# Kernel optimization log

Hardware: AMD Instinct MI355X
Metric: run time of the kernel (lower is better)

Reference implementation:

```python
import jax, jax.numpy as jnp
import numpy as np

MG = (5, 5)          # mesh_grid_size
UP = (17, 17)        # upsample_size
IMG = (512.0, 512.0) # image_size
B = 8192
FC_OUT = MG[0] * MG[1] * 2  # 50
KH = (UP[0] - 1) // (MG[0] - 1) + 1  # 5
KW = (UP[1] - 1) // (MG[1] - 1) + 1  # 5
SH = (UP[0] - 1) // (MG[0] - 1)      # 4
SW = (UP[1] - 1) // (MG[1] - 1)      # 4
L0 = MG[0] - 1
L1 = MG[1] - 1


def _grid(h, w):
    # channel 0: x coords vary along rows (image_size[0]); channel 1: y along cols
    x_t = jnp.broadcast_to(jnp.linspace(0.0, IMG[0], h)[:, None], (h, w))
    y_t = jnp.broadcast_to(jnp.linspace(0.0, IMG[1], w)[None, :], (h, w))
    return jnp.stack([x_t, y_t], 0)  # [2, h, w]


def _unfold22(a):
    # a: [B, 2, H, W] -> [B, (H-1)*(W-1), 4, 2]; 4 = kernel positions row-major, 2 = channel
    p = jnp.stack([a[:, :, :-1, :-1], a[:, :, :-1, 1:],
                   a[:, :, 1:, :-1], a[:, :, 1:, 1:]], axis=2)  # [B,2,4,H-1,W-1]
    return p.reshape(a.shape[0], 2, 4, -1).transpose(0, 3, 2, 1)


def _persp(src, dst):
    # exact 4-point homography solve (torchgeometry.get_perspective_transform)
    x0, y0 = src[..., 0], src[..., 1]
    u, v = dst[..., 0], dst[..., 1]
    z = jnp.zeros_like(x0)
    o = jnp.ones_like(x0)
    ax = jnp.stack([x0, y0, o, z, z, z, -u * x0, -u * y0], -1)  # [N,4,8]
    ay = jnp.stack([z, z, z, x0, y0, o, -v * x0, -v * y0], -1)
    A = jnp.concatenate([ax, ay], 1)                 # [N,8,8]
    bb = jnp.concatenate([u, v], 1)[..., None]       # [N,8,1]
    h = jnp.linalg.solve(A, bb)[..., 0]              # [N,8]
    return jnp.concatenate([h, o[:, :1]], 1).reshape(-1, 3, 3)


def setup_inputs() -> dict:
    key = jax.random.key(0)
    ks = jax.random.split(key, 4)
    def lin(k, i, o):
        return jax.random.normal(k, (i, o), jnp.float32) / jnp.sqrt(i)
    return {
        "x": jax.random.normal(ks[0], (B, 1024), jnp.float32),
        "W1": lin(ks[1], 1024, 1024), "b1": jnp.zeros((1024,), jnp.float32),
        "W2": lin(ks[2], 1024, 2048), "b2": jnp.zeros((2048,), jnp.float32),
        "W3": lin(ks[3], 2048, FC_OUT), "b3": jnp.zeros((FC_OUT,), jnp.float32),
    }


def reference(x, W1, b1, W2, b2, W3, b3):
    Bn = x.shape[0]
    h = jax.nn.relu(x @ W1 + b1)
    h = jax.nn.relu(h @ W2 + b2)
    out = (h @ W3 + b3).reshape(Bn, 2, MG[0], MG[1])  # [B,2,5,5] mesh flow

    # sparse control grid and 2x2 patch corner points
    gs = _grid(MG[0], MG[1])
    src = _unfold22(jnp.broadcast_to(gs[None], (Bn, 2, MG[0], MG[1]))).reshape(-1, 4, 2)
    flow = _unfold22(out).reshape(-1, 4, 2)
    M = _persp(src, src + flow)  # [B*16, 3, 3]

    # dense grid and its unfold2 (kernel KHxKW, stride SHxSW) patch points
    gd = _grid(UP[0], UP[1])  # [2, 17, 17]
    gi = (np.arange(L0) * SH)[:, None, None, None] + np.arange(KH)[None, None, :, None]
    gj = (np.arange(L1) * SW)[None, :, None, None] + np.arange(KW)[None, None, None, :]
    I, J = np.broadcast_arrays(gi, gj)  # [L0,L1,KH,KW]
    pts = gd[:, I, J].transpose(1, 2, 3, 4, 0).reshape(1, L0 * L1, KH * KW, 2)
    pts = jnp.broadcast_to(pts, (Bn, L0 * L1, KH * KW, 2)).reshape(Bn * L0 * L1, KH * KW, 2)

    # transform_points: homogeneous warp + perspective divide
    ph = jnp.concatenate([pts, jnp.ones(pts.shape[:-1] + (1,), pts.dtype)], -1)
    oh = jnp.einsum('nij,npj->npi', M, ph)
    warped = oh[..., :2] / oh[..., 2:3]
    warped = warped.reshape(Bn, L0, L1, KH, KW, 2)

    # Fold: scatter-accumulate overlapping patches
    fold = jnp.zeros((Bn, 2, UP[0], UP[1]), x.dtype)
    for i in range(L0):
        for j in range(L1):
            blk = warped[:, i, j].transpose(0, 3, 1, 2)  # [B,2,KH,KW]
            fold = fold.at[:, :, i * SH:i * SH + KH, j * SW:j * SW + KW].add(blk)

    # boundary rescaling exactly as the torch code: only the 5x5 crossing points
    idx = np.arange(0, UP[0], MG[0] - 1)
    X, Y = np.meshgrid(idx, idx, indexing='xy')
    fold = fold.at[:, :, X, Y].multiply(0.5)
    for (a, b) in ((0, 0), (0, UP[1] - 1), (UP[0] - 1, UP[1] - 1), (UP[0] - 1, 0)):
        fold = fold.at[:, :, a, b].multiply(2.0)

    return fold - gd[None]  # upsampled mesh flow [B,2,17,17]
```

## Files before the change

### kernel.cpp

```cpp
#include <hip/hip_runtime.h>

typedef __bf16 bf16x8 __attribute__((ext_vector_type(8)));
typedef float f32x4 __attribute__((ext_vector_type(4)));

__device__ __forceinline__ unsigned short f2bf(float f) {
  unsigned int u = __builtin_bit_cast(unsigned int, f);
  unsigned int r = (u + 0x7fffu + ((u >> 16) & 1u)) >> 16;
  return (unsigned short)r;
}

__device__ __forceinline__ float bf2f(unsigned short u) {
  unsigned int v = ((unsigned int)u) << 16;
  return __builtin_bit_cast(float, v);
}

__device__ __forceinline__ void load16_lds(const unsigned short* g, unsigned short* l) {
  __builtin_amdgcn_global_load_lds(
      (const __attribute__((address_space(1))) void*)g,
      (__attribute__((address_space(3))) void*)l, 16, 0, 0);
}

__device__ __forceinline__ void wait_vm0() {
  asm volatile("s_waitcnt vmcnt(0)" ::: "memory");
  __builtin_amdgcn_sched_barrier(0);
}
__device__ __forceinline__ void barrier_raw() {
  __builtin_amdgcn_sched_barrier(0);
  __builtin_amdgcn_s_barrier();
  __builtin_amdgcn_sched_barrier(0);
}


__global__ __launch_bounds__(256) void prepass(
    const float* __restrict__ x, const float* __restrict__ W1,
    const float* __restrict__ W2, const float* __restrict__ W3,
    unsigned short* __restrict__ xbf, unsigned short* __restrict__ w1t,
    unsigned short* __restrict__ w2t, unsigned short* __restrict__ w3t) {
  __shared__ float tile[32][33];
  const int bid = blockIdx.x;
  const int t = threadIdx.x;
  if (bid < 2048) {
    for (int i = bid * 256 + t; i < 2097152; i += 2048 * 256) {
      float4 f = ((const float4*)x)[i];
      uint2 o;
      o.x = (unsigned)f2bf(f.x) | ((unsigned)f2bf(f.y) << 16);
      o.y = (unsigned)f2bf(f.z) | ((unsigned)f2bf(f.w) << 16);
      ((uint2*)xbf)[i] = o;
    }
  } else if (bid < 3072) {
    int ti = bid - 2048;
    int n0 = (ti & 31) * 32, k0 = (ti >> 5) * 32;
    int tx = t & 31, ty = t >> 5;
    #pragma unroll
    for (int r = 0; r < 32; r += 8)
      tile[ty + r][tx] = W1[(size_t)(k0 + ty + r) * 1024 + n0 + tx];
    __syncthreads();
    #pragma unroll
    for (int r = 0; r < 32; r += 8)
      w1t[(size_t)(n0 + ty + r) * 1024 + k0 + tx] = f2bf(tile[tx][ty + r]);
  } else if (bid < 5120) {
    int ti = bid - 3072;
    int n0 = (ti & 63) * 32, k0 = (ti >> 6) * 32;
    int tx = t & 31, ty = t >> 5;
    #pragma unroll
    for (int r = 0; r < 32; r += 8)
      tile[ty + r][tx] = W2[(size_t)(k0 + ty + r) * 2048 + n0 + tx];
    __syncthreads();
    #pragma unroll
    for (int r = 0; r < 32; r += 8)
      w2t[(size_t)(n0 + ty + r) * 1024 + k0 + tx] = f2bf(tile[tx][ty + r]);
  } else {
    int idx = (bid - 5120) * 256 + t;
    int n = idx >> 11, k = idx & 2047;
    w3t[idx] = f2bf((n < 50) ? W3[(size_t)k * 50 + n] : 0.f);
  }
}


__global__ __launch_bounds__(256, 2) void gemm1_v8(
    const unsigned short* __restrict__ A,
    const unsigned short* __restrict__ Bt,
    const float* __restrict__ bias,
    unsigned short* __restrict__ C) {
  constexpr int K = 1024, N = 1024, NT = 16;
  constexpr int AEL = 128 * 64;
  constexpr int BUF = 2 * AEL;
  __shared__ __align__(16) unsigned short smem[2 * BUF];
  const int t = threadIdx.x;
  const int m0 = blockIdx.x * 128;
  const int n0 = blockIdx.y * 128;
  const int lane = t & 63, wv = t >> 6;
  const int l16 = lane & 15, quad = lane >> 4;
  const int rb = (wv >> 1) * 64, cb = (wv & 1) * 64;

  const int srow = t >> 3;
  const int sg = ((t & 7) ^ (srow & 7)) * 8;
  const unsigned short* Ag0 = A + (size_t)(m0 + srow) * K + sg;
  const unsigned short* Bg0 = Bt + (size_t)(n0 + srow) * K + sg;
  const int ldsO = wv * 8 * 64;

  f32x4 acc[4][4] = {};

  #pragma unroll
  for (int r = 0; r < 4; ++r) {
    load16_lds(Ag0 + (size_t)(r * 32) * K, &smem[r * 2048 + ldsO]);
    load16_lds(Bg0 + (size_t)(r * 32) * K, &smem[AEL + r * 2048 + ldsO]);
  }

  for (int kt = 0; kt < NT; ++kt) {
    unsigned short* Ls = &smem[(kt & 1) * BUF];

    wait_vm0();
    barrier_raw();

    if (kt + 1 < NT) {
      unsigned short* Ln = &smem[((kt + 1) & 1) * BUF];
      const unsigned short* An = Ag0 + (size_t)(kt + 1) * 64;
      const unsigned short* Bn = Bg0 + (size_t)(kt + 1) * 64;
      #pragma unroll
      for (int r = 0; r < 4; ++r) {
        load16_lds(An + (size_t)(r * 32) * K, &Ln[r * 2048 + ldsO]);
        load16_lds(Bn + (size_t)(r * 32) * K, &Ln[AEL + r * 2048 + ldsO]);
      }
    }

    #pragma unroll
    for (int half = 0; half < 2; ++half) {
      bf16x8 af[4], bfr[4];
      #pragma unroll
      for (int ni = 0; ni < 4; ++ni) {
        int row = cb + ni * 16 + l16;
        bfr[ni] = *(const bf16x8*)&Ls[AEL + row * 64 + ((half * 4 + quad) ^ (row & 7)) * 8];
      }
      #pragma unroll
      for (int mi = 0; mi < 4; ++mi) {
        int row = rb + mi * 16 + l16;
        af[mi] = *(const bf16x8*)&Ls[row * 64 + ((half * 4 + quad) ^ (row & 7)) * 8];
      }
      #pragma unroll
      for (int mi = 0; mi < 4; ++mi)
        #pragma unroll
        for (int ni = 0; ni < 4; ++ni)
          acc[mi][ni] = __builtin_amdgcn_mfma_f32_16x16x32_bf16(
              af[mi], bfr[ni], acc[mi][ni], 0, 0, 0);
    }
  }
  barrier_raw();

  unsigned short* Cs = smem;
  float bv[4];
  #pragma unroll
  for (int ni = 0; ni < 4; ++ni) bv[ni] = bias[n0 + cb + ni * 16 + l16];
  #pragma unroll
  for (int mi = 0; mi < 4; ++mi)
    #pragma unroll
    for (int ni = 0; ni < 4; ++ni)
      #pragma unroll
      for (int r = 0; r < 4; ++r) {
        int row = rb + mi * 16 + quad * 4 + r;
        int col = cb + ni * 16 + l16;
        int pb = (col >> 3) ^ (row & 15);
        Cs[row * 128 + pb * 8 + (col & 7)] = f2bf(fmaxf(acc[mi][ni][r] + bv[ni], 0.f));
      }
  __syncthreads();
  #pragma unroll
  for (int j = 0; j < 8; ++j) {
    int idx = j * 256 + t;
    int row = idx >> 4, cg = idx & 15;
    int pb = cg ^ (row & 15);
    *(uint4*)&C[(size_t)(m0 + row) * N + n0 + cg * 8] =
        *(const uint4*)&Cs[row * 128 + pb * 8];
  }
}


__global__ __launch_bounds__(512, 4) void gemm2_v8(
    const unsigned short* __restrict__ A,
    const unsigned short* __restrict__ Bt,
    const float* __restrict__ bias,
    const unsigned short* __restrict__ W3t,
    unsigned short* __restrict__ part) {
  constexpr int K = 1024, NT = 32;
  constexpr int AEL = 256 * 32;
  constexpr int BEL = 128 * 32;
  constexpr int BUF = AEL + BEL;
  __shared__ __align__(16) unsigned short smem[32768];
  const int t = threadIdx.x;
  const int m0 = blockIdx.x * 256;
  const int n0 = blockIdx.y * 128;
  const int lane = t & 63, wv = t >> 6;
  const int l16 = lane & 15, quad = lane >> 4;
  const int rb = (wv >> 1) * 64, cb = (wv & 1) * 64;

  const int tr = t >> 2;
  const int cg = ((t & 3) - (tr >> 1)) & 3;
  const unsigned short* Ag0 = A + (size_t)(m0 + tr) * K + cg * 8;
  const unsigned short* Bg0 = Bt + (size_t)(n0 + tr) * K + cg * 8;
  const int ldsO = wv * 512;

  f32x4 acc[4][4] = {};

  load16_lds(Ag0, &smem[ldsO]);
  load16_lds(Ag0 + (size_t)128 * K, &smem[4096 + ldsO]);
  load16_lds(Bg0, &smem[AEL + ldsO]);

  for (int kt = 0; kt < NT; ++kt) {
    unsigned short* Ls = &smem[(kt & 1) * BUF];

    wait_vm0();
    barrier_raw();

    if (kt + 1 < NT) {
      unsigned short* Ln = &smem[((kt + 1) & 1) * BUF];
      const unsigned short* An = Ag0 + (size_t)(kt + 1) * 32;
      const unsigned short* Bn = Bg0 + (size_t)(kt + 1) * 32;
      load16_lds(An, &Ln[ldsO]);
      load16_lds(An + (size_t)128 * K, &Ln[4096 + ldsO]);
      load16_lds(Bn, &Ln[AEL + ldsO]);
    }

    bf16x8 af[4], bfr[4];
    #pragma unroll
    for (int ni = 0; ni < 4; ++ni) {
      int row = cb + ni * 16 + l16;
      bfr[ni] = *(const bf16x8*)&Ls[AEL + row * 32 + ((quad + (row >> 1)) & 3) * 8];
    }
    #pragma unroll
    for (int mi = 0; mi < 4; ++mi) {
      int row = rb + mi * 16 + l16;
      af[mi] = *(const bf16x8*)&Ls[row * 32 + ((quad + (row >> 1)) & 3) * 8];
    }
    #pragma unroll
    for (int mi = 0; mi < 4; ++mi)
      #pragma unroll
      for (int ni = 0; ni < 4; ++ni)
        acc[mi][ni] = __builtin_amdgcn_mfma_f32_16x16x32_bf16(
            af[mi], bfr[ni], acc[mi][ni], 0, 0, 0);
  }
  barrier_raw();

  unsigned short* Cs = smem;
  float bv[4];
  #pragma unroll
  for (int ni = 0; ni < 4; ++ni) bv[ni] = bias[n0 + cb + ni * 16 + l16];
  #pragma unroll
  for (int mi = 0; mi < 4; ++mi)
    #pragma unroll
    for (int ni = 0; ni < 4; ++ni)
      #pragma unroll
      for (int r = 0; r < 4; ++r) {
        int row = rb + mi * 16 + quad * 4 + r;
        int col = cb + ni * 16 + l16;
        int pb = (col >> 3) ^ (row & 15);
        Cs[row * 128 + pb * 8 + (col & 7)] = f2bf(fmaxf(acc[mi][ni][r] + bv[ni], 0.f));
      }
  __syncthreads();

  bf16x8 bq[4][4];
  #pragma unroll
  for (int ks = 0; ks < 4; ++ks)
    #pragma unroll
    for (int nt = 0; nt < 4; ++nt)
      bq[ks][nt] = *(const bf16x8*)&W3t[(size_t)(nt * 16 + l16) * 2048 +
                                        n0 + ks * 32 + quad * 8];
  f32x4 acc2[2][4] = {};
  #pragma unroll
  for (int ks = 0; ks < 4; ++ks) {
    bf16x8 af2[2];
    #pragma unroll
    for (int mt = 0; mt < 2; ++mt) {
      int row = wv * 32 + mt * 16 + l16;
      int pb = (ks * 4 + quad) ^ (row & 15);
      af2[mt] = *(const bf16x8*)&Cs[row * 128 + pb * 8];
    }
    #pragma unroll
    for (int mt = 0; mt < 2; ++mt)
      #pragma unroll
      for (int nt = 0; nt < 4; ++nt)
        acc2[mt][nt] = __builtin_amdgcn_mfma_f32_16x16x32_bf16(
            af2[mt], bq[ks][nt], acc2[mt][nt], 0, 0, 0);
  }

  const int zi = blockIdx.y;
  #pragma unroll
  for (int mt = 0; mt < 2; ++mt)
    #pragma unroll
    for (int nt = 0; nt < 4; ++nt) {
      int col = nt * 16 + l16;
      #pragma unroll
      for (int r = 0; r < 4; ++r) {
        int row = m0 + wv * 32 + mt * 16 + quad * 4 + r;
        part[((size_t)row * 16 + zi) * 64 + col] = f2bf(acc2[mt][nt][r]);
      }
    }
}


__global__ __launch_bounds__(256) void geom_reduce(
    const unsigned short* __restrict__ part,
    const float* __restrict__ b3,
    float* __restrict__ outp) {
  __shared__ float s_out3[16 * 64];
  __shared__ float unfold[16][16][50];
  const int t = threadIdx.x;
  const int bbase = blockIdx.x * 16;

  for (int i = t; i < 1024; i += 256) {
    int m = i >> 6, n = i & 63;
    const unsigned short* p = part + ((size_t)(bbase + m) * 16) * 64 + n;
    float v = 0.f;
    #pragma unroll
    for (int z = 0; z < 16; ++z) v += bf2f(p[z * 64]);
    s_out3[i] = v + ((n < 50) ? b3[n] : 0.f);
  }
  __syncthreads();

  {
    const int bl = t >> 4;
    const int p = t & 15;
    const int pi = p >> 2, pj = p & 3;
    const float* o = &s_out3[bl * 64];

    float u00 = 128.f * pi       + o[pi * 5 + pj];
    float v00 = 128.f * pj       + o[25 + pi * 5 + pj];
    float u01 = 128.f * pi       + o[pi * 5 + pj + 1];
    float v01 = 128.f * (pj + 1) + o[25 + pi * 5 + pj + 1];
    float u10 = 128.f * (pi + 1) + o[(pi + 1) * 5 + pj];
    float v10 = 128.f * pj       + o[25 + (pi + 1) * 5 + pj];
    float u11 = 128.f * (pi + 1) + o[(pi + 1) * 5 + pj + 1];
    float v11 = 128.f * (pj + 1) + o[25 + (pi + 1) * 5 + pj + 1];

    float sx = u00 - u10 + u11 - u01;
    float sy = v00 - v10 + v11 - v01;
    float dx1 = u10 - u11, dx2 = u01 - u11;
    float dy1 = v10 - v11, dy2 = v01 - v11;
    float rden = 1.f / (dx1 * dy2 - dx2 * dy1);
    float g = (sx * dy2 - dx2 * sy) * rden;
    float h = (dx1 * sy - sx * dy1) * rden;
    float a = u10 - u00 + g * u10;
    float b = u01 - u00 + h * u01;
    float c = u00;
    float d = v10 - v00 + g * v10;
    float e = v01 - v00 + h * v01;
    float f = v00;

    #pragma unroll
    for (int ai = 0; ai < 5; ++ai) {
      #pragma unroll
      for (int bi = 0; bi < 5; ++bi) {
        float s = 0.25f * ai, tt = 0.25f * bi;
        float rw = 1.f / (g * s + h * tt + 1.f);
        unfold[bl][p][ai * 5 + bi]      = (a * s + b * tt + c) * rw;
        unfold[bl][p][25 + ai * 5 + bi] = (d * s + e * tt + f) * rw;
      }
    }
  }
  __syncthreads();

  for (int i = t; i < 16 * 578; i += 256) {
    int blb = i / 578;
    int rem = i - blb * 578;
    int ch = rem / 289;
    int ij = rem - ch * 289;
    int gi = ij / 17, gj = ij - gi * 17;

    int pi0 = (gi == 16) ? 3 : (gi >> 2);
    int ai0 = gi - 4 * pi0;
    int ci = (((gi & 3) == 0) && gi != 0 && gi != 16) ? 2 : 1;
    int pj0 = (gj == 16) ? 3 : (gj >> 2);
    int bj0 = gj - 4 * pj0;
    int cj = (((gj & 3) == 0) && gj != 0 && gj != 16) ? 2 : 1;

    float val = 0.f;
    #pragma unroll
    for (int ii = 0; ii < 2; ++ii) {
      if (ii < ci) {
        int pi = pi0 - ii, ai = ii ? 4 : ai0;
        #pragma unroll
        for (int jj = 0; jj < 2; ++jj) {
          if (jj < cj) {
            int pj = pj0 - jj, bi = jj ? 4 : bj0;
            val += unfold[blb][pi * 4 + pj][ch * 25 + ai * 5 + bi];
          }
        }
      }
    }

    if (((gi & 3) == 0) && ((gj & 3) == 0)) val *= 0.5f;
    if ((gi == 0 || gi == 16) && (gj == 0 || gj == 16)) val *= 2.f;
    val -= (ch == 0) ? 32.f * gi : 32.f * gj;
    outp[(size_t)(bbase + blb) * 578 + rem] = val;
  }
}


extern "C" void kernel_launch(void* const* d_in, const int* in_sizes, int n_in,
                              void* d_out, int out_size, void* d_ws, size_t ws_size,
                              hipStream_t stream) {
  const float* x  = (const float*)d_in[0];
  const float* W1 = (const float*)d_in[1];
  const float* b1 = (const float*)d_in[2];
  const float* W2 = (const float*)d_in[3];
  const float* b2 = (const float*)d_in[4];
  const float* W3 = (const float*)d_in[5];
  const float* b3 = (const float*)d_in[6];
  float* outp = (float*)d_out;

  char* ws = (char*)d_ws;
  unsigned short* xbf = (unsigned short*)ws;
  unsigned short* w1t = (unsigned short*)(ws + (size_t)16 * 1024 * 1024);
  unsigned short* part = (unsigned short*)ws;
  unsigned short* w2t = (unsigned short*)(ws + (size_t)34 * 1024 * 1024);
  unsigned short* w3t = (unsigned short*)(ws + (size_t)38 * 1024 * 1024);
  unsigned short* h1  = (unsigned short*)(ws + (size_t)38 * 1024 * 1024 + 512 * 1024);

  prepass<<<5632, 256, 0, stream>>>(x, W1, W2, W3, xbf, w1t, w2t, w3t);

  gemm1_v8<<<dim3(64, 8), 256, 0, stream>>>(xbf, w1t, b1, h1);
  gemm2_v8<<<dim3(32, 16), 512, 0, stream>>>(h1, w2t, b2, w3t, part);
  geom_reduce<<<512, 256, 0, stream>>>(part, b3, outp);
}
```

Before: 184.1 us.

## Restructure gemm1 to 512 threads with K-tile 32 and new LDS swizzle

Rewrites the first GEMM kernel to use 512 threads per block (8 waves, each computing 32x64) instead of 256 threads (4 waves, 64x64). The K tile drops from 64 to 32, so LDS per block halves and the kernel runs twice as many K iterations, with a new rotation-based LDS swizzle. The intent is more waves in flight and higher occupancy to hide memory latency. In exchange each wave reuses fewer A fragments per B load, and there are twice as many barriers per block.

Result: no change. 181.5 us (-1.4%).

```diff
diff --git a/kernel.cpp b/kernel.cpp
--- a/kernel.cpp
+++ b/kernel.cpp
@@ -77,13 +77,13 @@
 }
 
 
-__global__ __launch_bounds__(256, 2) void gemm1_v8(
+__global__ __launch_bounds__(512, 4) void gemm1_v9(
     const unsigned short* __restrict__ A,
     const unsigned short* __restrict__ Bt,
     const float* __restrict__ bias,
     unsigned short* __restrict__ C) {
-  constexpr int K = 1024, N = 1024, NT = 16;
-  constexpr int AEL = 128 * 64;
+  constexpr int K = 1024, N = 1024, NT = 32;
+  constexpr int AEL = 128 * 32;
   constexpr int BUF = 2 * AEL;
   __shared__ __align__(16) unsigned short smem[2 * BUF];
   const int t = threadIdx.x;
@@ -91,21 +91,18 @@
   const int n0 = blockIdx.y * 128;
   const int lane = t & 63, wv = t >> 6;
   const int l16 = lane & 15, quad = lane >> 4;
-  const int rb = (wv >> 1) * 64, cb = (wv & 1) * 64;
-
-  const int srow = t >> 3;
-  const int sg = ((t & 7) ^ (srow & 7)) * 8;
-  const unsigned short* Ag0 = A + (size_t)(m0 + srow) * K + sg;
-  const unsigned short* Bg0 = Bt + (size_t)(n0 + srow) * K + sg;
-  const int ldsO = wv * 8 * 64;
-
-  f32x4 acc[4][4] = {};
-
-  #pragma unroll
-  for (int r = 0; r < 4; ++r) {
-    load16_lds(Ag0 + (size_t)(r * 32) * K, &smem[r * 2048 + ldsO]);
-    load16_lds(Bg0 + (size_t)(r * 32) * K, &smem[AEL + r * 2048 + ldsO]);
-  }
+  const int rb = (wv >> 1) * 32, cb = (wv & 1) * 64;
+
+  const int tr = t >> 2;
+  const int cg = ((t & 3) - (tr >> 1)) & 3;
+  const unsigned short* Ag0 = A + (size_t)(m0 + tr) * K + cg * 8;
+  const unsigned short* Bg0 = Bt + (size_t)(n0 + tr) * K + cg * 8;
+  const int ldsO = wv * 512;
+
+  f32x4 acc[2][4] = {};
+
+  load16_lds(Ag0, &smem[ldsO]);
+  load16_lds(Bg0, &smem[AEL + ldsO]);
 
   for (int kt = 0; kt < NT; ++kt) {
     unsigned short* Ls = &smem[(kt & 1) * BUF];
@@ -115,35 +112,27 @@
 
     if (kt + 1 < NT) {
       unsigned short* Ln = &smem[((kt + 1) & 1) * BUF];
-      const unsigned short* An = Ag0 + (size_t)(kt + 1) * 64;
-      const unsigned short* Bn = Bg0 + (size_t)(kt + 1) * 64;
-      #pragma unroll
-      for (int r = 0; r < 4; ++r) {
-        load16_lds(An + (size_t)(r * 32) * K, &Ln[r * 2048 + ldsO]);
-        load16_lds(Bn + (size_t)(r * 32) * K, &Ln[AEL + r * 2048 + ldsO]);
-      }
-    }
-
-    #pragma unroll
-    for (int half = 0; half < 2; ++half) {
-      bf16x8 af[4], bfr[4];
-      #pragma unroll
-      for (int ni = 0; ni < 4; ++ni) {
-        int row = cb + ni * 16 + l16;
-        bfr[ni] = *(const bf16x8*)&Ls[AEL + row * 64 + ((half * 4 + quad) ^ (row & 7)) * 8];
-      }
-      #pragma unroll
-      for (int mi = 0; mi < 4; ++mi) {
-        int row = rb + mi * 16 + l16;
-        af[mi] = *(const bf16x8*)&Ls[row * 64 + ((half * 4 + quad) ^ (row & 7)) * 8];
-      }
-      #pragma unroll
-      for (int mi = 0; mi < 4; ++mi)
-        #pragma unroll
-        for (int ni = 0; ni < 4; ++ni)
-          acc[mi][ni] = __builtin_amdgcn_mfma_f32_16x16x32_bf16(
-              af[mi], bfr[ni], acc[mi][ni], 0, 0, 0);
-    }
+      load16_lds(Ag0 + (size_t)(kt + 1) * 32, &Ln[ldsO]);
+      load16_lds(Bg0 + (size_t)(kt + 1) * 32, &Ln[AEL + ldsO]);
+    }
+
+    bf16x8 af[2], bfr[4];
+    #pragma unroll
+    for (int ni = 0; ni < 4; ++ni) {
+      int row = cb + ni * 16 + l16;
+      bfr[ni] = *(const bf16x8*)&Ls[AEL + row * 32 + ((quad + (row >> 1)) & 3) * 8];
+    }
+    #pragma unroll
+    for (int mi = 0; mi < 2; ++mi) {
+      int row = rb + mi * 16 + l16;
+      af[mi] = *(const bf16x8*)&Ls[row * 32 + ((quad + (row >> 1)) & 3) * 8];
+    }
+    #pragma unroll
+    for (int mi = 0; mi < 2; ++mi)
+      #pragma unroll
+      for (int ni = 0; ni < 4; ++ni)
+        acc[mi][ni] = __builtin_amdgcn_mfma_f32_16x16x32_bf16(
+            af[mi], bfr[ni], acc[mi][ni], 0, 0, 0);
   }
   barrier_raw();
 
@@ -152,7 +141,7 @@
   #pragma unroll
   for (int ni = 0; ni < 4; ++ni) bv[ni] = bias[n0 + cb + ni * 16 + l16];
   #pragma unroll
-  for (int mi = 0; mi < 4; ++mi)
+  for (int mi = 0; mi < 2; ++mi)
     #pragma unroll
     for (int ni = 0; ni < 4; ++ni)
       #pragma unroll
@@ -164,11 +153,11 @@
       }
   __syncthreads();
   #pragma unroll
-  for (int j = 0; j < 8; ++j) {
-    int idx = j * 256 + t;
-    int row = idx >> 4, cg = idx & 15;
-    int pb = cg ^ (row & 15);
-    *(uint4*)&C[(size_t)(m0 + row) * N + n0 + cg * 8] =
+  for (int j = 0; j < 4; ++j) {
+    int idx = j * 512 + t;
+    int row = idx >> 4, cgc = idx & 15;
+    int pb = cgc ^ (row & 15);
+    *(uint4*)&C[(size_t)(m0 + row) * N + n0 + cgc * 8] =
         *(const uint4*)&Cs[row * 128 + pb * 8];
   }
 }
@@ -416,7 +405,7 @@
 
   prepass<<<5632, 256, 0, stream>>>(x, W1, W2, W3, xbf, w1t, w2t, w3t);
 
-  gemm1_v8<<<dim3(64, 8), 256, 0, stream>>>(xbf, w1t, b1, h1);
+  gemm1_v9<<<dim3(64, 8), 512, 0, stream>>>(xbf, w1t, b1, h1);
   gemm2_v8<<<dim3(32, 16), 512, 0, stream>>>(h1, w2t, b2, w3t, part);
   geom_reduce<<<512, 256, 0, stream>>>(part, b3, outp);
 }
```
